# Kernel optimization log

Hardware: AMD Instinct MI355X
Metric: run time of the kernel (lower is better)

## Reference

```python
import jax, jax.numpy as jnp
import numpy as np

B, N, D, H, E = 4, 2048, 512, 8, 512   # batch, seq, d_model, heads, dpb_embedding
D1 = 2 * D                              # expand_ratio * d_model (multiple of H)
HD = D1 // H                            # head dim for v/u space
GAMMA = 0.999


def _srms(x):
    # SimpleRMSNorm: x / (||x|| * d^-0.5 + eps)
    return x / (jnp.sqrt(jnp.mean(jnp.square(x), axis=-1, keepdims=True)) + 1e-8)


def setup_inputs() -> dict:
    key = jax.random.key(0)
    ks = jax.random.split(key, 10)
    s = 0.02

    def lin(k, i, o):
        kw, kb = jax.random.split(k)
        return (jax.random.normal(kw, (i, o), jnp.float32) * s,
                jax.random.normal(kb, (o,), jnp.float32) * s)

    Wu, bu = lin(ks[0], D, D1)
    Wv, bv = lin(ks[1], D, D1)
    Wo, bo = lin(ks[2], D1, D)
    Wp, bp = lin(ks[3], 1, E)        # DPB pos_proj: scalar position -> dpb_dim
    W1, b1 = lin(ks[4], E, E)
    W2, b2 = lin(ks[5], E, E)
    W3, b3 = lin(ks[6], E, E)
    Wz, bz = lin(ks[7], E, H * HD)   # DPB out: dpb_dim -> h*head_dim
    x = jax.random.normal(ks[8], (B, N, D), jnp.float32)
    return dict(x=x, Wu=Wu, bu=bu, Wv=Wv, bv=bv, Wo=Wo, bo=bo,
                Wp=Wp, bp=bp, W1=W1, b1=b1, W2=W2, b2=b2, W3=W3, b3=b3,
                Wz=Wz, bz=bz)


def reference(x, Wu, bu, Wv, bv, Wo, bo, Wp, bp, W1, b1, W2, b2, W3, b3, Wz, bz):
    shortcut = x                       # token_shift_type=-1, resi_param=False
    xn = _srms(x)                      # pre_norm = SimpleRMSNorm(d_model)
    u = jax.nn.silu(xn @ Wu + bu)      # b n d1
    v = jax.nn.silu(xn @ Wv + bv)      # b n d1
    b, n, _ = x.shape
    v = v.reshape(b, n, H, HD).transpose(0, 2, 1, 3)   # b h n d

    # --- DPB (Rpe MLP) on positions [0, 1, ..., n-1]; row 0 is the zero lag ---
    pos = jnp.arange(0, n, dtype=x.dtype).reshape(n, 1)  # par_type=1
    hcf = pos @ Wp + bp
    for W, bb in ((W1, b1), (W2, b2), (W3, b3)):         # non-residual layers
        hcf = jax.nn.relu(_srms(hcf)) @ W + bb
    coef = jax.nn.relu(_srms(hcf)) @ Wz + bz             # n, h*d
    coef = coef.reshape(n, H, HD).transpose(1, 0, 2)     # h n d
    zero = coef[:, :1]                                   # h 1 d  (lag 0)
    posc = coef[:, 1:]                                   # h n-1 d (lags 1..n-1)

    # fixed exponential decay gamma^i on positive lags (use_decay=True)
    decay = GAMMA ** jnp.arange(1, n, dtype=x.dtype)[None, :, None]
    # causal: negative lags are zero; rfft zero-pads to 2n
    a = jnp.concatenate([zero, decay * posc, zero], axis=1)  # h, n+1, d

    # --- causal Toeplitz matmul as circular conv of length 2n ---
    m = 2 * n
    fv = jnp.fft.rfft(v, m, axis=2)           # b h m/2+1 d
    fa = jnp.fft.rfft(a, m, axis=1)[None]     # 1 h m/2+1 d
    out = jnp.fft.irfft(fv * fa, m, axis=2)[:, :, :n]  # b h n d

    out = out.transpose(0, 2, 1, 3).reshape(b, n, H * HD)  # b n d1
    out = u * out                               # u-gating
    return out @ Wo + bo + shortcut             # output proj + residual
```

## Files before the change

### kernel.cpp

```cpp
#include <hip/hip_runtime.h>
#include <hip/hip_bf16.h>
#include <math.h>

using bf16 = __hip_bfloat16;
typedef short bf16x8 __attribute__((ext_vector_type(8)));
typedef float f32x4 __attribute__((ext_vector_type(4)));

#define GAMMA_LOG2 (-0.0014434688536725045f)

union Bf16Bits { bf16 h; unsigned short s; };
union VecU { uint4 q; unsigned short s[8]; };

__device__ inline unsigned short bf16_bits(float z)
{
    Bf16Bits u;
    u.h = __float2bfloat16(z);
    return u.s;
}

__device__ inline unsigned int packbf2(float a, float b)
{
    return (unsigned int)bf16_bits(a) | ((unsigned int)bf16_bits(b) << 16);
}

struct PrepArgs {
    const float* src[3];
    bf16* dst[3];
    int R[3];
    int C[3];
    int pfx[4];
};

__global__ void k_prep(PrepArgs pa)
{
    __shared__ float tile[32][33];
    int bid = blockIdx.x;
    int seg = 0;
    while (bid >= pa.pfx[seg + 1]) ++seg;
    int local = bid - pa.pfx[seg];
    int R = pa.R[seg], C = pa.C[seg];
    int ctiles = C >> 5;
    int c0 = (local % ctiles) * 32, r0 = (local / ctiles) * 32;
    const float* in = pa.src[seg];
    bf16* out = pa.dst[seg];
    int tx = threadIdx.x & 31, ty = threadIdx.x >> 5;
#pragma unroll
    for (int i = 0; i < 4; ++i) {
        int r = r0 + ty + 8 * i;
        tile[ty + 8 * i][tx] = in[(size_t)r * C + c0 + tx];
    }
    __syncthreads();
#pragma unroll
    for (int i = 0; i < 4; ++i) {
        int cc = c0 + ty + 8 * i, rr = r0 + tx;
        out[(size_t)cc * R + rr] = __float2bfloat16(tile[tx][ty + 8 * i]);
    }
}

__global__ void k_prep_mlp(const float* __restrict__ W1, const float* __restrict__ W2,
                           const float* __restrict__ W3, const float* __restrict__ Wz,
                           bf16* __restrict__ Wf)
{
    int g = blockIdx.x * 256 + threadIdx.x;
    int unit = g >> 15;
    int idx = g & 32767;
    int lane = idx & 63;
    int nj = (idx >> 6) & 7;
    int ks = (idx >> 9) & 15;
    int wc = idx >> 13;
    int lm = lane & 15, lq = lane >> 4;
    int k0 = ks * 32 + lq * 8;
    const float* src;
    int N, o;
    if (unit < 3) {
        src = (unit == 0) ? W1 : (unit == 1) ? W2 : W3;
        N = 512;
        o = wc * 128 + nj * 16 + lm;
    } else {
        src = Wz;
        N = 1024;
        o = (unit - 3) * 512 + wc * 128 + nj * 16 + lm;
    }
    VecU v;
#pragma unroll
    for (int j = 0; j < 8; ++j)
        v.s[j] = bf16_bits(src[(size_t)(k0 + j) * N + o]);
    *(uint4*)(void*)(Wf + (size_t)g * 8) = v.q;
}

__global__ void k_transpose5(const bf16* __restrict__ uvb, const bf16* __restrict__ ab,
                             bf16* __restrict__ vtb, bf16* __restrict__ atb)
{
    __shared__ unsigned short tile[64][65];
    const int z = blockIdx.z;
    const bf16* in;
    bf16* out;
    int in_stride, col0;
    if (z < 4) {
        in = uvb + (size_t)z * 2048 * 2048;
        out = vtb + (size_t)z * 1024 * 2048;
        in_stride = 2048;
        col0 = 1024;
    } else {
        in = ab;
        out = atb;
        in_stride = 1024;
        col0 = 0;
    }
    const int t = threadIdx.x;
    int c0 = blockIdx.x * 64, r0 = blockIdx.y * 64;
#pragma unroll
    for (int it = 0; it < 2; ++it) {
        int r = it * 32 + (t >> 3), cc = (t & 7) * 8;
        VecU v;
        v.q = *(const uint4*)(const void*)(in + (size_t)(r0 + r) * in_stride + col0 + c0 + cc);
#pragma unroll
        for (int i = 0; i < 8; ++i) tile[r][cc + i] = v.s[i];
    }
    __syncthreads();
#pragma unroll
    for (int it = 0; it < 2; ++it) {
        int c = it * 32 + (t >> 3), rr = (t & 7) * 8;
        VecU v;
#pragma unroll
        for (int i = 0; i < 8; ++i) v.s[i] = tile[rr + i][c];
        *(uint4*)(void*)(out + (size_t)(c0 + c) * 2048 + r0 + rr) = v.q;
    }
}

__global__ void k_gate_transpose(const bf16* __restrict__ ud1t, const bf16* __restrict__ uv,
                                 bf16* __restrict__ out)
{
    __shared__ float tile[32][33];
    const int b = blockIdx.z;
    int c0 = blockIdx.x * 32, t0 = blockIdx.y * 32;
    int tx = threadIdx.x & 31, ty = threadIdx.x >> 5;
#pragma unroll
    for (int i = 0; i < 4; ++i) {
        int cc = c0 + ty + 8 * i;
        tile[ty + 8 * i][tx] = __bfloat162float(ud1t[((size_t)b * 1024 + cc) * 2048 + t0 + tx]);
    }
    __syncthreads();
#pragma unroll
    for (int i = 0; i < 4; ++i) {
        int t = t0 + ty + 8 * i, c = c0 + tx;
        float u = __bfloat162float(uv[((size_t)b * 2048 + t) * 2048 + c]);
        out[((size_t)b * 2048 + t) * 1024 + c] = __float2bfloat16(tile[tx][ty + 8 * i] * u);
    }
}

__global__ void k_rms_x(const float* __restrict__ x, bf16* __restrict__ xn)
{
    int row = blockIdx.x, t = threadIdx.x;
    const float* xr = x + (size_t)row * 512;
    float a = xr[t], b = xr[t + 256];
    float v = a * a + b * b;
#pragma unroll
    for (int m = 32; m >= 1; m >>= 1) v += __shfl_xor(v, m, 64);
    __shared__ float ws[4];
    if ((t & 63) == 0) ws[t >> 6] = v;
    __syncthreads();
    float tot = ws[0] + ws[1] + ws[2] + ws[3];
    float s = 1.f / (sqrtf(tot * (1.f / 512.f)) + 1e-8f);
    bf16* o = xn + (size_t)row * 512;
    o[t] = __float2bfloat16(a * s);
    o[t + 256] = __float2bfloat16(b * s);
}

struct SharedUV {
    union {
        struct { unsigned short As[128 * 40]; unsigned short Bs[128 * 40]; } g;
        struct {
            unsigned short X[32][520];
            float sq[16][17];
            float red[4][32];
            float scale[32];
        } m;
    };
};

__global__ __launch_bounds__(256, 2) void k_uv_mlp(
    const bf16* __restrict__ A, const bf16* __restrict__ Bt,
    const float* __restrict__ bu, const float* __restrict__ bv,
    const float* __restrict__ Wp, const float* __restrict__ bp,
    const bf16* __restrict__ Wf,
    const float* __restrict__ b1, const float* __restrict__ b2,
    const float* __restrict__ b3, const float* __restrict__ bz,
    bf16* __restrict__ uvb, bf16* __restrict__ ab)
{
    __shared__ SharedUV sh;

    const int tid = threadIdx.x, lane = tid & 63, w = tid >> 6;
    const int lm = lane & 15, lq = lane >> 4;

    if (blockIdx.x < 64) {
        unsigned short (&X)[32][520] = sh.m.X;
        float (&sq)[16][17] = sh.m.sq;
        float (&red)[4][32] = sh.m.red;
        float (&scale)[32] = sh.m.scale;

        const int posBase = blockIdx.x * 32;

#pragma unroll
        for (int hf = 0; hf < 2; ++hf) {
            const int rl = tid >> 4;
            const int r = hf * 16 + rl;
            const int c0 = (tid & 15) * 32;
            float vals[32];
            float ssq = 0.f;
            const float fp = (float)(posBase + r);
#pragma unroll
            for (int e = 0; e < 32; ++e) {
                float z = fp * Wp[c0 + e] + bp[c0 + e];
                vals[e] = z;
                ssq += z * z;
            }
            sq[rl][tid & 15] = ssq;
            __syncthreads();
            float tot = 0.f;
#pragma unroll
            for (int i = 0; i < 16; ++i) tot += sq[rl][i];
            float s = 1.f / (sqrtf(tot * (1.f / 512.f)) + 1e-8f);
            unsigned int* xrow = (unsigned int*)&X[r][c0];
#pragma unroll
            for (int e = 0; e < 16; ++e)
                xrow[e] = packbf2(fmaxf(vals[2 * e] * s, 0.f), fmaxf(vals[2 * e + 1] * s, 0.f));
            __syncthreads();
        }

        auto layer_mm = [&](const bf16* Wu_, f32x4 (&acc)[2][8]) {
            const bf16* base = Wu_ + (size_t)w * 65536 + (size_t)lane * 8;
            bf16x8 bufB[3][8];
#pragma unroll
            for (int d = 0; d < 2; ++d)
#pragma unroll
                for (int nj = 0; nj < 8; ++nj)
                    bufB[d][nj] = *(const bf16x8*)(const void*)(base + d * 4096 + nj * 512);
#pragma unroll
            for (int ks = 0; ks < 16; ++ks) {
                const int cb = ks % 3;
                if (ks < 14) {
                    const int pf = (ks + 2) % 3;
#pragma unroll
                    for (int nj = 0; nj < 8; ++nj)
                        bufB[pf][nj] = *(const bf16x8*)(const void*)(base + (ks + 2) * 4096 + nj * 512);
                }
                bf16x8 af0 = *(const bf16x8*)(const void*)&X[lm][ks * 32 + lq * 8];
                bf16x8 af1 = *(const bf16x8*)(const void*)&X[16 + lm][ks * 32 + lq * 8];
#pragma unroll
                for (int nj = 0; nj < 8; ++nj) {
                    acc[0][nj] = __builtin_amdgcn_mfma_f32_16x16x32_bf16(af0, bufB[cb][nj], acc[0][nj], 0, 0, 0);
                    acc[1][nj] = __builtin_amdgcn_mfma_f32_16x16x32_bf16(af1, bufB[cb][nj], acc[1][nj], 0, 0, 0);
                }
            }
        };

        const float* bs[3] = {b1, b2, b3};
        for (int l = 0; l < 3; ++l) {
            f32x4 acc[2][8];
#pragma unroll
            for (int mi = 0; mi < 2; ++mi)
#pragma unroll
                for (int i = 0; i < 8; ++i) acc[mi][i] = (f32x4){0.f, 0.f, 0.f, 0.f};
            layer_mm(Wf + (size_t)l * 262144, acc);
#pragma unroll
            for (int mi = 0; mi < 2; ++mi)
#pragma unroll
                for (int nj = 0; nj < 8; ++nj) {
                    float bb = bs[l][w * 128 + nj * 16 + lm];
#pragma unroll
                    for (int r = 0; r < 4; ++r) acc[mi][nj][r] += bb;
                }
            float pr[2][4] = {{0.f, 0.f, 0.f, 0.f}, {0.f, 0.f, 0.f, 0.f}};
#pragma unroll
            for (int mi = 0; mi < 2; ++mi)
#pragma unroll
                for (int nj = 0; nj < 8; ++nj)
#pragma unroll
                    for (int r = 0; r < 4; ++r) pr[mi][r] += acc[mi][nj][r] * acc[mi][nj][r];
#pragma unroll
            for (int m = 1; m < 16; m <<= 1)
#pragma unroll
                for (int mi = 0; mi < 2; ++mi)
#pragma unroll
                    for (int r = 0; r < 4; ++r) pr[mi][r] += __shfl_xor(pr[mi][r], m);
            if (lm == 0)
#pragma unroll
                for (int mi = 0; mi < 2; ++mi)
#pragma unroll
                    for (int r = 0; r < 4; ++r) red[w][mi * 16 + lq * 4 + r] = pr[mi][r];
            __syncthreads();
            if (tid < 32) {
                float tot = red[0][tid] + red[1][tid] + red[2][tid] + red[3][tid];
                scale[tid] = 1.f / (sqrtf(tot * (1.f / 512.f)) + 1e-8f);
            }
            __syncthreads();
#pragma unroll
            for (int mi = 0; mi < 2; ++mi)
#pragma unroll
                for (int nj = 0; nj < 8; ++nj) {
                    int col = w * 128 + nj * 16 + lm;
#pragma unroll
                    for (int r = 0; r < 4; ++r) {
                        int row = mi * 16 + lq * 4 + r;
                        float z = fmaxf(acc[mi][nj][r] * scale[row], 0.f);
                        *(unsigned short*)&X[row][col] = bf16_bits(z);
                    }
                }
            __syncthreads();
        }

#pragma unroll
        for (int h = 0; h < 2; ++h) {
            f32x4 acc[2][8];
#pragma unroll
            for (int mi = 0; mi < 2; ++mi)
#pragma unroll
                for (int i = 0; i < 8; ++i) acc[mi][i] = (f32x4){0.f, 0.f, 0.f, 0.f};
            layer_mm(Wf + (size_t)(3 + h) * 262144, acc);
#pragma unroll
            for (int mi = 0; mi < 2; ++mi)
#pragma unroll
                for (int nj = 0; nj < 8; ++nj) {
                    int col = h * 512 + w * 128 + nj * 16 + lm;
                    float bb = bz[col];
#pragma unroll
                    for (int r = 0; r < 4; ++r) {
                        int pos = posBase + mi * 16 + lq * 4 + r;
                        float z = (acc[mi][nj][r] + bb) * exp2f((float)pos * GAMMA_LOG2);
                        ab[(size_t)pos * 1024 + col] = __float2bfloat16(z);
                    }
                }
        }
        return;
    }

    unsigned short* As = sh.g.As;
    unsigned short* Bs = sh.g.Bs;

    const int gid = (int)blockIdx.x - 64;
    const int wm = (w >> 1) * 64, wn = (w & 1) * 64;
    const long rowBase = (long)(gid & 63) * 128, colBase = (long)(gid >> 6) * 128;

    f32x4 acc[4][4];
    f32x4 zz = {0.f, 0.f, 0.f, 0.f};
#pragma unroll
    for (int i = 0; i < 4; ++i)
#pragma unroll
        for (int j = 0; j < 4; ++j) acc[i][j] = zz;

    for (int k0 = 0; k0 < 512; k0 += 32) {
#pragma unroll
        for (int i = 0; i < 2; ++i) {
            int idx = (i * 256 + tid) * 8;
            int r = idx >> 5, kk = idx & 31;
            *(uint4*)(void*)(As + r * 40 + kk) =
                *(const uint4*)(const void*)(A + (rowBase + r) * 512 + k0 + kk);
        }
#pragma unroll
        for (int i = 0; i < 2; ++i) {
            int idx = (i * 256 + tid) * 8;
            int r = idx >> 5, kk = idx & 31;
            *(uint4*)(void*)(Bs + r * 40 + kk) =
                *(const uint4*)(const void*)(Bt + (colBase + r) * 512 + k0 + kk);
        }
        __syncthreads();
        bf16x8 af[4], bfr[4];
#pragma unroll
        for (int mi = 0; mi < 4; ++mi)
            af[mi] = *(const bf16x8*)(const void*)(As + (wm + mi * 16 + lm) * 40 + lq * 8);
#pragma unroll
        for (int nj = 0; nj < 4; ++nj)
            bfr[nj] = *(const bf16x8*)(const void*)(Bs + (wn + nj * 16 + lm) * 40 + lq * 8);
#pragma unroll
        for (int mi = 0; mi < 4; ++mi)
#pragma unroll
            for (int nj = 0; nj < 4; ++nj)
                acc[mi][nj] = __builtin_amdgcn_mfma_f32_16x16x32_bf16(af[mi], bfr[nj], acc[mi][nj], 0, 0, 0);
        __syncthreads();
    }

#pragma unroll
    for (int mi = 0; mi < 4; ++mi)
#pragma unroll
        for (int nj = 0; nj < 4; ++nj) {
            long col = colBase + wn + nj * 16 + lm;
            float bb = (col < 1024) ? bu[col] : bv[col - 1024];
#pragma unroll
            for (int r = 0; r < 4; ++r) {
                long row = rowBase + wm + mi * 16 + lq * 4 + r;
                float z = acc[mi][nj][r] + bb;
                z = z / (1.f + __expf(-z));
                uvb[(size_t)row * 2048 + col] = __float2bfloat16(z);
            }
        }
}

template <int BM, int BN, int WM, int WN>
__global__ __launch_bounds__(256, 2) void k_gemm_out(
    const bf16* __restrict__ A, const bf16* __restrict__ Bt,
    const float* __restrict__ bias0, const float* __restrict__ addsrc,
    float* __restrict__ outp, int M, int N, int K)
{
    constexpr int BK = 32, LDT = BK + 8;
    constexpr int MI = WM / 16, NJ = WN / 16;
    constexpr int WCOLS = BN / WN;
    __shared__ unsigned short As[BM * LDT];
    __shared__ unsigned short Bs[BN * LDT];
    const int tid = threadIdx.x;
    const int lane = tid & 63, w = tid >> 6;
    const int wm = (w / WCOLS) * WM, wn = (w % WCOLS) * WN;
    const int lm = lane & 15, lq = lane >> 4;
    const long rowBase = (long)blockIdx.x * BM, colBase = (long)blockIdx.y * BN;

    f32x4 acc[MI][NJ];
    f32x4 zz = {0.f, 0.f, 0.f, 0.f};
#pragma unroll
    for (int i = 0; i < MI; ++i)
#pragma unroll
        for (int j = 0; j < NJ; ++j) acc[i][j] = zz;

    for (int k0 = 0; k0 < K; k0 += BK) {
#pragma unroll
        for (int i = 0; i < BM / 64; ++i) {
            int idx = (i * 256 + tid) * 8;
            int r = idx >> 5, kk = idx & 31;
            *(uint4*)(void*)(As + r * LDT + kk) =
                *(const uint4*)(const void*)(A + (rowBase + r) * K + k0 + kk);
        }
#pragma unroll
        for (int i = 0; i < BN / 64; ++i) {
            int idx = (i * 256 + tid) * 8;
            int r = idx >> 5, kk = idx & 31;
            *(uint4*)(void*)(Bs + r * LDT + kk) =
                *(const uint4*)(const void*)(Bt + (colBase + r) * K + k0 + kk);
        }
        __syncthreads();
        bf16x8 af[MI], bfr[NJ];
#pragma unroll
        for (int mi = 0; mi < MI; ++mi)
            af[mi] = *(const bf16x8*)(const void*)(As + (wm + mi * 16 + lm) * LDT + lq * 8);
#pragma unroll
        for (int nj = 0; nj < NJ; ++nj)
            bfr[nj] = *(const bf16x8*)(const void*)(Bs + (wn + nj * 16 + lm) * LDT + lq * 8);
#pragma unroll
        for (int mi = 0; mi < MI; ++mi)
#pragma unroll
            for (int nj = 0; nj < NJ; ++nj)
                acc[mi][nj] = __builtin_amdgcn_mfma_f32_16x16x32_bf16(af[mi], bfr[nj], acc[mi][nj], 0, 0, 0);
        __syncthreads();
    }

#pragma unroll
    for (int mi = 0; mi < MI; ++mi)
#pragma unroll
        for (int nj = 0; nj < NJ; ++nj) {
            long col = colBase + wn + nj * 16 + lm;
#pragma unroll
            for (int r = 0; r < 4; ++r) {
                long row = rowBase + wm + mi * 16 + lq * 4 + r;
                size_t off = (size_t)row * N + col;
                outp[off] = acc[mi][nj][r] + bias0[col] + addsrc[off];
            }
        }
}

__global__ __launch_bounds__(256, 4) void k_conv_mfma(
    const bf16* __restrict__ vt, const bf16* __restrict__ at, bf16* __restrict__ ud1t)
{
    __shared__ unsigned short ash2[2][2068];
    __shared__ unsigned short vsh[4][3072];

    const int tid = threadIdx.x, lane = tid & 63, w = tid >> 6;
    const int c = blockIdx.x;

    {
        const unsigned short* asrc = (const unsigned short*)(at + (size_t)c * 2048);
        for (int i = tid; i < 2068; i += 256) {
#pragma unroll
            for (int k = 0; k < 2; ++k) {
                int src = 2047 - i - k;
                ash2[k][i] = (src >= 0) ? asrc[src] : (unsigned short)0;
            }
        }
    }
    {
        const bf16* vsrc = vt + ((size_t)w * 1024 + c) * 2048;
#pragma unroll
        for (int q = 0; q < 4; ++q) {
            int li = q * 64 + lane;
            int tile = li >> 1, hf = li & 1;
            *(uint4*)(void*)&vsh[w][tile * 24 + hf * 8] =
                *(const uint4*)(const void*)(vsrc + li * 8);
        }
    }
    __syncthreads();

    const int lm = lane & 15, lq = lane >> 4;
    const int h = lq >> 1, p0 = (lq & 1) * 8;
    const int kcopy = (lm + 1) & 1;
    const int base = 31 - 16 * h - lm + p0 - kcopy;
    const unsigned int* aw = (const unsigned int*)(void*)&ash2[kcopy][0] + (base >> 1);
    const unsigned short* vw = &vsh[w][0];

    f32x4 acc[8];
    f32x4 zz = {0.f, 0.f, 0.f, 0.f};
#pragma unroll
    for (int i = 0; i < 8; ++i) acc[i] = zz;
    const bf16x8 zfrag = (bf16x8)(short)0;

    for (int d2 = 0; d2 < 16; d2 += 2) {
        bf16x8 vf[8];
        const int tb = lm - d2 - h;
        {
            int T = tb > 0 ? tb : 0;
            bf16x8 f = *(const bf16x8*)(const void*)(vw + T * 24 + p0);
            vf[0] = (tb < 0) ? zfrag : f;
        }
#pragma unroll
        for (int dl = 1; dl < 8; ++dl)
            vf[dl] = *(const bf16x8*)(const void*)(vw + (dl * 16 + tb) * 24 + p0);

#pragma unroll
        for (int dt = 0; dt < 8; ++dt) {
            const int m16 = (63 - ((dt * 16 + d2) >> 1)) * 16;
            union { unsigned int u[4]; bf16x8 v; } af;
            af.u[0] = aw[m16 + 0];
            af.u[1] = aw[m16 + 1];
            af.u[2] = aw[m16 + 2];
            af.u[3] = aw[m16 + 3];
#pragma unroll
            for (int dl = 0; dl < 8 - dt; ++dl)
                acc[dt + dl] = __builtin_amdgcn_mfma_f32_16x16x32_bf16(af.v, vf[dl], acc[dt + dl], 0, 0, 0);
        }
    }

    __syncthreads();
    float* stg = (float*)(void*)((char*)(void*)&ash2[0][0] + w * 1024);
    bf16* dst = ud1t + ((size_t)w * 1024 + c) * 2048;
#pragma unroll
    for (int jg = 0; jg < 8; ++jg) {
        *(f32x4*)(void*)&stg[lm * 16 + lq * 4] = acc[jg];
        f32x4 vv = *(const f32x4*)(const void*)&stg[lane * 4];
        uint2 o;
        o.x = packbf2(vv.x, vv.y);
        o.y = packbf2(vv.z, vv.w);
        *(uint2*)(void*)(dst + jg * 256 + lane * 4) = o;
    }
}

extern "C" void kernel_launch(void* const* d_in, const int* in_sizes, int n_in,
                              void* d_out, int out_size, void* d_ws, size_t ws_size,
                              hipStream_t stream)
{
    const float* x  = (const float*)d_in[0];
    const float* Wu = (const float*)d_in[1];
    const float* bu = (const float*)d_in[2];
    const float* Wv = (const float*)d_in[3];
    const float* bv = (const float*)d_in[4];
    const float* Wo = (const float*)d_in[5];
    const float* bo = (const float*)d_in[6];
    const float* Wp = (const float*)d_in[7];
    const float* bp = (const float*)d_in[8];
    const float* W1 = (const float*)d_in[9];
    const float* b1 = (const float*)d_in[10];
    const float* W2 = (const float*)d_in[11];
    const float* b2 = (const float*)d_in[12];
    const float* W3 = (const float*)d_in[13];
    const float* b3 = (const float*)d_in[14];
    const float* Wz = (const float*)d_in[15];
    const float* bz = (const float*)d_in[16];

    char* p = (char*)d_ws;
    auto carve = [&](size_t bytes) { void* q = (void*)p; p += (bytes + 255) & ~(size_t)255; return q; };
    bf16*  xn   = (bf16*)carve((size_t)8192 * 512 * 2);
    bf16*  Wuvt = (bf16*)carve((size_t)2048 * 512 * 2);
    bf16*  Wot  = (bf16*)carve((size_t)512 * 1024 * 2);
    bf16*  Wf   = (bf16*)carve((size_t)5 * 262144 * 2);
    bf16*  uvb  = (bf16*)carve((size_t)8192 * 2048 * 2);
    bf16*  ud1  = (bf16*)carve((size_t)8192 * 1024 * 2);
    bf16*  ab   = (bf16*)carve((size_t)2048 * 1024 * 2);
    bf16*  vtb  = (bf16*)carve((size_t)4 * 1024 * 2048 * 2);
    bf16*  atb  = (bf16*)carve((size_t)1024 * 2048 * 2);
    bf16*  ud1t = (bf16*)carve((size_t)4 * 1024 * 2048 * 2);

    PrepArgs pa;
    const float* srcs[3] = {Wu, Wv, Wo};
    bf16* dsts[3] = {Wuvt, Wuvt + (size_t)1024 * 512, Wot};
    int Rs[3] = {512, 512, 1024};
    int Cs[3] = {1024, 1024, 512};
    int acc_t = 0;
    for (int i = 0; i < 3; ++i) {
        pa.src[i] = srcs[i]; pa.dst[i] = dsts[i]; pa.R[i] = Rs[i]; pa.C[i] = Cs[i];
        pa.pfx[i] = acc_t;
        acc_t += (Rs[i] / 32) * (Cs[i] / 32);
    }
    pa.pfx[3] = acc_t;
    k_prep<<<acc_t, 256, 0, stream>>>(pa);

    k_prep_mlp<<<640, 256, 0, stream>>>(W1, W2, W3, Wz, Wf);

    k_rms_x<<<8192, 256, 0, stream>>>(x, xn);

    k_uv_mlp<<<1088, 256, 0, stream>>>(xn, Wuvt, bu, bv, Wp, bp,
                                       Wf, b1, b2, b3, bz, uvb, ab);

    k_transpose5<<<dim3(16, 32, 5), 256, 0, stream>>>(uvb, ab, vtb, atb);

    k_conv_mfma<<<dim3(1024), 256, 0, stream>>>(vtb, atb, ud1t);

    k_gate_transpose<<<dim3(32, 64, 4), 256, 0, stream>>>(ud1t, uvb, ud1);

    k_gemm_out<128, 128, 64, 64><<<dim3(64, 4), 256, 0, stream>>>(
        ud1, Wot, bo, x, (float*)d_out, 8192, 512, 1024);
}
```

Baseline: 248.8 us.

## Double-buffer uv GEMM tiles via async global-to-LDS loads with XOR swizzle

The uv projection GEMM now streams its A and B tiles with global_load_lds (16-byte direct-to-LDS copies) into a double-buffered, XOR-swizzled LDS layout. The next k-slice is prefetched while MFMAs run on the current one, and one barrier per iteration replaces the two-barrier load/compute loop. The DPB MLP weight prefetch drops from a 3-deep to a 2-deep register ring, which lowers register pressure but shortens prefetch distance. Risks include correctness of waits on the async LDS writes, since only __syncthreads is used, and LDS bank behaviour of the swizzle.

```diff
diff --git a/kernel.cpp b/kernel.cpp
--- a/kernel.cpp
+++ b/kernel.cpp
@@ -21,6 +21,14 @@
 __device__ inline unsigned int packbf2(float a, float b)
 {
     return (unsigned int)bf16_bits(a) | ((unsigned int)bf16_bits(b) << 16);
+}
+
+__device__ __forceinline__ void async_copy16(unsigned short* lds, const bf16* g)
+{
+    __builtin_amdgcn_global_load_lds(
+        (const __attribute__((address_space(1))) unsigned int*)(const void*)g,
+        (__attribute__((address_space(3))) unsigned int*)(void*)lds,
+        16, 0, 0);
 }
 
 struct PrepArgs {
@@ -169,7 +177,7 @@
 
 struct SharedUV {
     union {
-        struct { unsigned short As[128 * 40]; unsigned short Bs[128 * 40]; } g;
+        struct { unsigned short AB[2][2][128 * 32]; } g;
         struct {
             unsigned short X[32][520];
             float sq[16][17];
@@ -230,20 +238,17 @@
 
         auto layer_mm = [&](const bf16* Wu_, f32x4 (&acc)[2][8]) {
             const bf16* base = Wu_ + (size_t)w * 65536 + (size_t)lane * 8;
-            bf16x8 bufB[3][8];
-#pragma unroll
-            for (int d = 0; d < 2; ++d)
-#pragma unroll
-                for (int nj = 0; nj < 8; ++nj)
-                    bufB[d][nj] = *(const bf16x8*)(const void*)(base + d * 4096 + nj * 512);
+            bf16x8 bufB[2][8];
+#pragma unroll
+            for (int nj = 0; nj < 8; ++nj)
+                bufB[0][nj] = *(const bf16x8*)(const void*)(base + nj * 512);
 #pragma unroll
             for (int ks = 0; ks < 16; ++ks) {
-                const int cb = ks % 3;
-                if (ks < 14) {
-                    const int pf = (ks + 2) % 3;
+                const int cb = ks & 1;
+                if (ks < 15) {
 #pragma unroll
                     for (int nj = 0; nj < 8; ++nj)
-                        bufB[pf][nj] = *(const bf16x8*)(const void*)(base + (ks + 2) * 4096 + nj * 512);
+                        bufB[cb ^ 1][nj] = *(const bf16x8*)(const void*)(base + (ks + 1) * 4096 + nj * 512);
                 }
                 bf16x8 af0 = *(const bf16x8*)(const void*)&X[lm][ks * 32 + lq * 8];
                 bf16x8 af1 = *(const bf16x8*)(const void*)&X[16 + lm][ks * 32 + lq * 8];
@@ -335,13 +340,24 @@
         return;
     }
 
-    unsigned short* As = sh.g.As;
-    unsigned short* Bs = sh.g.Bs;
+    unsigned short (&AB)[2][2][128 * 32] = sh.g.AB;
 
     const int gid = (int)blockIdx.x - 64;
     const int wm = (w >> 1) * 64, wn = (w & 1) * 64;
     const long rowBase = (long)(gid & 63) * 128, colBase = (long)(gid >> 6) * 128;
 
+    const int srow = tid >> 2;
+    const int sqz  = (tid & 3) ^ ((srow >> 1) & 3);
+    const bf16* gA  = A  + (rowBase + srow) * 512 + sqz * 8;
+    const bf16* gB  = Bt + (colBase + srow) * 512 + sqz * 8;
+    const bf16* gA2 = gA + (size_t)64 * 512;
+    const bf16* gB2 = gB + (size_t)64 * 512;
+    const int ls0 = w * 512;
+    const int ls1 = 2048 + w * 512;
+
+    const int rdA = ((wm + lm) * 4 + (lq ^ ((lm >> 1) & 3))) * 8;
+    const int rdB = ((wn + lm) * 4 + (lq ^ ((lm >> 1) & 3))) * 8;
+
     f32x4 acc[4][4];
     f32x4 zz = {0.f, 0.f, 0.f, 0.f};
 #pragma unroll
@@ -349,35 +365,35 @@
 #pragma unroll
         for (int j = 0; j < 4; ++j) acc[i][j] = zz;
 
-    for (int k0 = 0; k0 < 512; k0 += 32) {
-#pragma unroll
-        for (int i = 0; i < 2; ++i) {
-            int idx = (i * 256 + tid) * 8;
-            int r = idx >> 5, kk = idx & 31;
-            *(uint4*)(void*)(As + r * 40 + kk) =
-                *(const uint4*)(const void*)(A + (rowBase + r) * 512 + k0 + kk);
-        }
-#pragma unroll
-        for (int i = 0; i < 2; ++i) {
-            int idx = (i * 256 + tid) * 8;
-            int r = idx >> 5, kk = idx & 31;
-            *(uint4*)(void*)(Bs + r * 40 + kk) =
-                *(const uint4*)(const void*)(Bt + (colBase + r) * 512 + k0 + kk);
-        }
-        __syncthreads();
+    async_copy16(&AB[0][0][ls0], gA);
+    async_copy16(&AB[0][0][ls1], gA2);
+    async_copy16(&AB[0][1][ls0], gB);
+    async_copy16(&AB[0][1][ls1], gB2);
+    __syncthreads();
+
+#pragma unroll
+    for (int t = 0; t < 16; ++t) {
+        const int cur = t & 1;
+        if (t < 15) {
+            const int kk = (t + 1) * 32;
+            async_copy16(&AB[cur ^ 1][0][ls0], gA + kk);
+            async_copy16(&AB[cur ^ 1][0][ls1], gA2 + kk);
+            async_copy16(&AB[cur ^ 1][1][ls0], gB + kk);
+            async_copy16(&AB[cur ^ 1][1][ls1], gB2 + kk);
+        }
         bf16x8 af[4], bfr[4];
 #pragma unroll
         for (int mi = 0; mi < 4; ++mi)
-            af[mi] = *(const bf16x8*)(const void*)(As + (wm + mi * 16 + lm) * 40 + lq * 8);
+            af[mi] = *(const bf16x8*)(const void*)&AB[cur][0][rdA + mi * 512];
 #pragma unroll
         for (int nj = 0; nj < 4; ++nj)
-            bfr[nj] = *(const bf16x8*)(const void*)(Bs + (wn + nj * 16 + lm) * 40 + lq * 8);
+            bfr[nj] = *(const bf16x8*)(const void*)&AB[cur][1][rdB + nj * 512];
 #pragma unroll
         for (int mi = 0; mi < 4; ++mi)
 #pragma unroll
             for (int nj = 0; nj < 4; ++nj)
                 acc[mi][nj] = __builtin_amdgcn_mfma_f32_16x16x32_bf16(af[mi], bfr[nj], acc[mi][nj], 0, 0, 0);
-        __syncthreads();
+        if (t < 15) __syncthreads();
     }
 
 #pragma unroll
```

After: 250.3 us. About the same (+0.6%).
